# Kernel tuning notes

Measured on AMD Instinct MI355X. Metric: run time of the kernel, lower is better.

## Reference

```python
import jax, jax.numpy as jnp
import numpy as np

NG, ND = 50000, 20000
EG, ED = 300000, 150000
FG = FD = 256
H = 256
FC = 2048
B = 65536
EPS = 1e-5


def _lrelu(x):
    return jnp.where(x >= 0, x, 0.01 * x)


def _bn(x, g, b):
    # BatchNorm1d in training mode: biased batch stats over the node dim
    m = x.mean(axis=0)
    v = ((x - m) ** 2).mean(axis=0)
    return (x - m) * jax.lax.rsqrt(v + EPS) * g + b


def _gconv(x, edge_index, Wr, br, Ws, n_nodes):
    # PyG GraphConv: out = lin_rel(sum_{j->i} x_j) + lin_root(x_i)
    src, dst = edge_index[0], edge_index[1]
    agg = jax.ops.segment_sum(x[src], dst, num_segments=n_nodes)  # [N, in]
    return agg @ Wr + br + x @ Ws


def setup_inputs() -> dict:
    key = jax.random.key(0)
    ks = iter(jax.random.split(key, 64))
    d = {}
    d["gene_x"] = jax.random.normal(next(ks), (NG, FG), jnp.float32)
    d["disease_x"] = jax.random.normal(next(ks), (ND, FD), jnp.float32)
    d["gene_edge_index"] = jax.random.randint(next(ks), (2, EG), 0, NG, jnp.int32)
    d["disease_edge_index"] = jax.random.randint(next(ks), (2, ED), 0, ND, jnp.int32)
    d["batch_idx"] = jax.random.randint(next(ks), (B, 2), 0, ND, jnp.int32)

    def lin(fin, fout):
        s = 1.0 / np.sqrt(fin)
        W = jax.random.uniform(next(ks), (fin, fout), jnp.float32, -s, s)
        b = jax.random.uniform(next(ks), (fout,), jnp.float32, -s, s)
        return W, b

    for p, fin in (("g", FG), ("d", FD)):
        for i in range(3):
            f = fin if i == 0 else H
            Wr, br = lin(f, H)
            Ws, _ = lin(f, H)
            d[f"{p}{i}_Wr"], d[f"{p}{i}_br"], d[f"{p}{i}_Ws"] = Wr, br, Ws
            d[f"bn{p}{i}_g"] = jnp.ones((H,), jnp.float32)
            d[f"bn{p}{i}_b"] = jnp.zeros((H,), jnp.float32)
    d["lin1_W"], d["lin1_b"] = lin(2 * H, FC)
    d["lin2_W"], d["lin2_b"] = lin(FC, FC // 2)
    d["lin3_W"], d["lin3_b"] = lin(FC // 2, FC // 4)
    d["lin4_W"], d["lin4_b"] = lin(FC // 4, 2)
    return d


def reference(gene_x, disease_x, gene_edge_index, disease_edge_index, batch_idx,
              g0_Wr, g0_br, g0_Ws, g1_Wr, g1_br, g1_Ws, g2_Wr, g2_br, g2_Ws,
              d0_Wr, d0_br, d0_Ws, d1_Wr, d1_br, d1_Ws, d2_Wr, d2_br, d2_Ws,
              bng0_g, bng0_b, bng1_g, bng1_b, bng2_g, bng2_b,
              bnd0_g, bnd0_b, bnd1_g, bnd1_b, bnd2_g, bnd2_b,
              lin1_W, lin1_b, lin2_W, lin2_b, lin3_W, lin3_b, lin4_W, lin4_b):
    # gene tower
    g0 = _bn(_lrelu(_gconv(gene_x, gene_edge_index, g0_Wr, g0_br, g0_Ws, NG)), bng0_g, bng0_b)
    g1 = _bn(_lrelu(_gconv(g0, gene_edge_index, g1_Wr, g1_br, g1_Ws, NG)), bng1_g, bng1_b)
    g2 = _bn(_lrelu(_gconv(g1, gene_edge_index, g2_Wr, g2_br, g2_Ws, NG)), bng2_g, bng2_b)
    gene_out = 0.7 * g0 + 0.2 * g1 + 0.1 * g2
    # disease tower
    h0 = _bn(_lrelu(_gconv(disease_x, disease_edge_index, d0_Wr, d0_br, d0_Ws, ND)), bnd0_g, bnd0_b)
    h1 = _bn(_lrelu(_gconv(h0, disease_edge_index, d1_Wr, d1_br, d1_Ws, ND)), bnd1_g, bnd1_b)
    h2 = _bn(_lrelu(_gconv(h1, disease_edge_index, d2_Wr, d2_br, d2_Ws, ND)), bnd2_g, bnd2_b)
    dis_out = 0.7 * h0 + 0.2 * h1 + 0.1 * h2
    # pair gather + MLP head (dropout is identity in eval)
    x = jnp.concatenate([gene_out[batch_idx[:, 0]], dis_out[batch_idx[:, 1]]], axis=1)
    x = _lrelu(x @ lin1_W + lin1_b)
    x = _lrelu(x @ lin2_W + lin2_b)
    x = _lrelu(x @ lin3_W + lin3_b)
    return x @ lin4_W + lin4_b
```

## Files before the change

kernel.cpp:

```cpp
#include <hip/hip_runtime.h>
#include <hip/hip_bf16.h>
#include <cstdint>
#include <cstddef>

#define N_G 50000
#define N_D 20000
#define E_G 300000
#define E_D 150000
#define BATCH 65536

typedef _Float16 f16;
typedef _Float16 f16x8 __attribute__((ext_vector_type(8)));
typedef _Float16 f16x4 __attribute__((ext_vector_type(4)));
typedef float f32x4 __attribute__((ext_vector_type(4)));

__device__ __forceinline__ float clampf(float v) {
    return fminf(fmaxf(v, -60000.f), 60000.f);
}

__device__ __forceinline__ void gl_lds16(const void* g, void* l) {
    __builtin_amdgcn_global_load_lds(
        (const __attribute__((address_space(1))) unsigned int*)g,
        (__attribute__((address_space(3))) unsigned int*)l, 16, 0, 0);
}

__global__ __launch_bounds__(256) void gemm_f16(
    const f16* __restrict__ A,
    const int* __restrict__ bidx,
    const f16* __restrict__ geneT, const f16* __restrict__ disT, int rowBase,
    const f16* __restrict__ Bt, const float* __restrict__ bias,
    f16* __restrict__ C, int M, int N, int K, int relu, int CB, int RB,
    const float* __restrict__ W4, float* __restrict__ outF,
    float* __restrict__ stats)
{
    alignas(16) __shared__ f16 sA[128 * 64];
    alignas(16) __shared__ f16 sB[128 * 64];
    const int t = threadIdx.x;
    const int w = t >> 6, l = t & 63;
    const int wm = w >> 1, wn = w & 1;
    const int q = l >> 4, lr = l & 15;

    int flat = blockIdx.x;
    int cb, rb;
    if ((RB & 7) == 0) {
        int x = flat & 7, idx = flat >> 3;
        int Sx = RB >> 3;
        cb = idx % CB;
        rb = x * Sx + idx / CB;
    } else {
        cb = flat % CB;
        rb = flat / CB;
    }
    const int mBase = rb * 128, nBase = cb * 128;

    const int subrow = l >> 3;
    const int c = l & 7;
    const char* pA[4];
    const char* pD[4];
    const char* pB[4];
    const bool fused = (bidx != nullptr);
    const bool concat = (!fused && disT != nullptr);
    const bool twoSrc = fused || concat;
#pragma unroll
    for (int j = 0; j < 4; j++) {
        int seg = j * 4 + w;
        int lrow = seg * 8 + subrow;
        int coff = ((c ^ (lrow & 7)) << 4);
        if (fused) {
            int rg = rowBase + mBase + lrow;
            int gi = bidx[2 * rg], di = bidx[2 * rg + 1];
            pA[j] = (const char*)geneT + (size_t)gi * 512 + coff;
            pD[j] = (const char*)disT + (size_t)di * 512 + coff;
        } else if (concat) {
            int arow = mBase + lrow; if (arow > M - 1) arow = M - 1;
            pA[j] = (const char*)geneT + (size_t)arow * 512 + coff;
            pD[j] = (const char*)disT + (size_t)arow * 512 + coff;
        } else {
            int arow = mBase + lrow; if (arow > M - 1) arow = M - 1;
            pA[j] = (const char*)A + (size_t)arow * K * 2 + coff;
            pD[j] = nullptr;
        }
        int brow = nBase + lrow; if (brow > N - 1) brow = N - 1;
        pB[j] = (const char*)Bt + (size_t)brow * K * 2 + coff;
    }

    f32x4 acc[4][4] = {};

    for (int k0 = 0; k0 < K; k0 += 64) {
        __syncthreads();
#pragma unroll
        for (int j = 0; j < 4; j++) {
            int seg = j * 4 + w;
            const char* srcA;
            if (twoSrc)
                srcA = (k0 < 256) ? (pA[j] + (size_t)k0 * 2) : (pD[j] + (size_t)(k0 - 256) * 2);
            else
                srcA = pA[j] + (size_t)k0 * 2;
            gl_lds16(srcA, sA + seg * 512);
            gl_lds16(pB[j] + (size_t)k0 * 2, sB + seg * 512);
        }
        __syncthreads();
        f16x8 a0[4], a1[4], b0[4], b1[4];
#pragma unroll
        for (int i = 0; i < 4; i++) {
            int r = wm * 64 + i * 16 + lr;
            int rs = r * 64;
            int x0 = (q ^ (r & 7)) << 3;
            int x1 = ((4 + q) ^ (r & 7)) << 3;
            a0[i] = *(const f16x8*)(sA + rs + x0);
            a1[i] = *(const f16x8*)(sA + rs + x1);
        }
#pragma unroll
        for (int jj = 0; jj < 4; jj++) {
            int r = wn * 64 + jj * 16 + lr;
            int rs = r * 64;
            int x0 = (q ^ (r & 7)) << 3;
            int x1 = ((4 + q) ^ (r & 7)) << 3;
            b0[jj] = *(const f16x8*)(sB + rs + x0);
            b1[jj] = *(const f16x8*)(sB + rs + x1);
        }
#pragma unroll
        for (int i = 0; i < 4; i++)
#pragma unroll
            for (int jj = 0; jj < 4; jj++) {
                acc[i][jj] = __builtin_amdgcn_mfma_f32_16x16x32_f16(a0[i], b0[jj], acc[i][jj], 0, 0, 0);
                acc[i][jj] = __builtin_amdgcn_mfma_f32_16x16x32_f16(a1[i], b1[jj], acc[i][jj], 0, 0, 0);
            }
    }

    if (W4 != nullptr) {
        float w40[4], w41[4];
#pragma unroll
        for (int j = 0; j < 4; j++) {
            int col = nBase + wn * 64 + j * 16 + lr;
            w40[j] = W4[col * 2];
            w41[j] = W4[col * 2 + 1];
        }
#pragma unroll
        for (int i = 0; i < 4; i++) {
#pragma unroll
            for (int r = 0; r < 4; r++) {
                int row = mBase + wm * 64 + i * 16 + q * 4 + r;
                float s0 = 0.f, s1 = 0.f;
#pragma unroll
                for (int j = 0; j < 4; j++) {
                    int col = nBase + wn * 64 + j * 16 + lr;
                    float v = acc[i][j][r] + bias[col];
                    v = v >= 0.f ? v : 0.01f * v;
                    v = clampf(v);
                    s0 += v * w40[j];
                    s1 += v * w41[j];
                }
#pragma unroll
                for (int off = 1; off < 16; off <<= 1) {
                    s0 += __shfl_xor(s0, off);
                    s1 += __shfl_xor(s1, off);
                }
                if (lr == 0 && row < M) {
                    atomicAdd(&outF[(size_t)(rowBase + row) * 2], s0);
                    atomicAdd(&outF[(size_t)(rowBase + row) * 2 + 1], s1);
                }
            }
        }
        return;
    }

    __syncthreads();
    f16* lt = ((w >> 1) ? sB : sA) + (w & 1) * 4096;

    float bj[4];
#pragma unroll
    for (int j = 0; j < 4; j++)
        bj[j] = bias ? bias[nBase + wn * 64 + j * 16 + lr] : 0.f;

    float sj[4] = {0.f, 0.f, 0.f, 0.f}, s2j[4] = {0.f, 0.f, 0.f, 0.f};
#pragma unroll
    for (int i = 0; i < 4; i++)
#pragma unroll
        for (int j = 0; j < 4; j++) {
            int col = j * 16 + lr;
#pragma unroll
            for (int r = 0; r < 4; r++) {
                int row = i * 16 + q * 4 + r;
                float v = acc[i][j][r] + bj[j];
                if (relu) v = v >= 0.f ? v : 0.01f * v;
                v = clampf(v);
                if (stats && (mBase + wm * 64 + row) < M) { sj[j] += v; s2j[j] += v * v; }
                int cs = col ^ ((((row >> 2) & 3) << 4) ^ ((row & 3) << 3));
                lt[row * 64 + cs] = (f16)v;
            }
        }

    if (stats) {
#pragma unroll
        for (int j = 0; j < 4; j++) {
            float s = sj[j], s2 = s2j[j];
            s += __shfl_xor(s, 16); s2 += __shfl_xor(s2, 16);
            s += __shfl_xor(s, 32); s2 += __shfl_xor(s2, 32);
            if (q == 0) {
                int col = nBase + wn * 64 + j * 16 + lr;
                if (col < 256 && col < N) {
                    atomicAdd(&stats[col], s);
                    atomicAdd(&stats[256 + col], s2);
                }
            }
        }
    }
    __syncthreads();

    const int rr = l >> 3;
    const int c8 = l & 7;
#pragma unroll
    for (int it = 0; it < 8; it++) {
        int row = it * 8 + rr;
        int cs = (c8 * 8) ^ ((((row >> 2) & 3) << 4) ^ ((row & 3) << 3));
        f16x8 vv = *(const f16x8*)(lt + row * 64 + cs);
        int grow = mBase + wm * 64 + row;
        if (grow < M)
            *(f16x8*)(C + (size_t)grow * N + nBase + wn * 64 + c8 * 8) = vv;
    }
}

__global__ __launch_bounds__(512) void gemm256(
    const f16* __restrict__ A,
    const int* __restrict__ bidx,
    const f16* __restrict__ geneT, const f16* __restrict__ disT, int rowBase,
    const f16* __restrict__ Bt, const float* __restrict__ bias,
    f16* __restrict__ C, int M, int N, int K, int relu, int CB, int RB)
{
    alignas(16) __shared__ f16 sm[81920];
    const int t = threadIdx.x;
    const int w = t >> 6, l = t & 63;
    const int wm = w >> 2, wn = w & 3;
    const int q = l >> 4, lr = l & 15;

    int flat = blockIdx.x;
    int cb, rb;
    if ((RB & 7) == 0) {
        int x = flat & 7, idx = flat >> 3;
        int Sx = RB >> 3;
        cb = idx % CB;
        rb = x * Sx + idx / CB;
    } else {
        cb = flat % CB;
        rb = flat / CB;
    }
    const int mBase = rb * 256, nBase = cb * 256;

    const int subrow = l >> 3;
    const int c = l & 7;
    const bool gat = (bidx != nullptr);
    const char* pA[4];
    const char* pD[4];
    const char* pB[4];
#pragma unroll
    for (int jj = 0; jj < 4; jj++) {
        int arow = jj * 64 + w * 8 + subrow;
        int coff = ((c ^ (arow & 7)) << 4);
        if (gat) {
            int rg = rowBase + mBase + arow;
            int gi = bidx[2 * rg], di = bidx[2 * rg + 1];
            pA[jj] = (const char*)geneT + (size_t)gi * 512 + coff;
            pD[jj] = (const char*)disT + (size_t)di * 512 + coff;
        } else {
            int ga = mBase + arow; if (ga > M - 1) ga = M - 1;
            pA[jj] = (const char*)A + (size_t)ga * K * 2 + coff;
            pD[jj] = nullptr;
        }
        int gb = nBase + arow; if (gb > N - 1) gb = N - 1;
        pB[jj] = (const char*)Bt + (size_t)gb * K * 2 + coff;
    }

    f16* const smA = sm;
    f16* const smB = sm + 3 * 16384;

    auto stageA = [&](int abuf, int k0) {
        f16* bA = smA + abuf * 16384;
#pragma unroll
        for (int jj = 0; jj < 4; jj++) {
            int R0 = jj * 64 + w * 8;
            const char* srcA;
            if (gat)
                srcA = (k0 < 256) ? (pA[jj] + (size_t)k0 * 2) : (pD[jj] + (size_t)(k0 - 256) * 2);
            else
                srcA = pA[jj] + (size_t)k0 * 2;
            gl_lds16(srcA, bA + R0 * 64);
        }
    };
    auto stageB = [&](int bbuf, int k0) {
        f16* bB = smB + bbuf * 16384;
#pragma unroll
        for (int jj = 0; jj < 4; jj++) {
            int R0 = jj * 64 + w * 8;
            gl_lds16(pB[jj] + (size_t)k0 * 2, bB + R0 * 64);
        }
    };

    f32x4 acc[8][4] = {};
    const int nkt = K >> 6;

    stageA(0, 0);
    stageB(0, 0);
    if (nkt > 1) stageA(1, 64);

    for (int kt = 0; kt < nkt; kt++) {
        if (kt + 1 < nkt) stageB((kt + 1) & 1, (kt + 1) << 6);
        if (kt + 2 < nkt) stageA((kt + 2) % 3, (kt + 2) << 6);
        if (kt + 2 < nkt)      asm volatile("s_waitcnt vmcnt(12)" ::: "memory");
        else if (kt + 1 < nkt) asm volatile("s_waitcnt vmcnt(8)" ::: "memory");
        else                   asm volatile("s_waitcnt vmcnt(0)" ::: "memory");
        __builtin_amdgcn_s_barrier();
        __builtin_amdgcn_sched_barrier(0);
        const f16* bA = smA + (kt % 3) * 16384;
        const f16* bB = smB + (kt & 1) * 16384;
#pragma unroll
        for (int ks = 0; ks < 2; ks++) {
            f16x8 bf[4];
#pragma unroll
            for (int nf = 0; nf < 4; nf++) {
                int rB = wn * 64 + nf * 16 + lr;
                bf[nf] = *(const f16x8*)(bB + rB * 64 + ((((ks << 2) + q) ^ (rB & 7)) << 3));
            }
#pragma unroll
            for (int mf = 0; mf < 8; mf++) {
                int rA = wm * 128 + mf * 16 + lr;
                f16x8 af = *(const f16x8*)(bA + rA * 64 + ((((ks << 2) + q) ^ (rA & 7)) << 3));
#pragma unroll
                for (int nf = 0; nf < 4; nf++)
                    acc[mf][nf] = __builtin_amdgcn_mfma_f32_16x16x32_f16(af, bf[nf], acc[mf][nf], 0, 0, 0);
            }
        }
        __builtin_amdgcn_sched_barrier(0);
        __builtin_amdgcn_s_barrier();
    }
    __builtin_amdgcn_sched_barrier(0);

    f16* lt = sm + w * 8192;
    float bj[4];
#pragma unroll
    for (int nf = 0; nf < 4; nf++)
        bj[nf] = bias ? bias[nBase + wn * 64 + nf * 16 + lr] : 0.f;

#pragma unroll
    for (int mf = 0; mf < 8; mf++)
#pragma unroll
        for (int nf = 0; nf < 4; nf++) {
            int col = nf * 16 + lr;
#pragma unroll
            for (int r = 0; r < 4; r++) {
                int row = mf * 16 + q * 4 + r;
                float v = acc[mf][nf][r] + bj[nf];
                if (relu) v = v >= 0.f ? v : 0.01f * v;
                v = clampf(v);
                int cs = col ^ ((((row >> 2) & 3) << 4) ^ ((row & 3) << 3));
                lt[row * 64 + cs] = (f16)v;
            }
        }

    const int rr = l >> 3;
    const int c8 = l & 7;
#pragma unroll
    for (int it = 0; it < 16; it++) {
        int row = it * 8 + rr;
        int cs = (c8 * 8) ^ ((((row >> 2) & 3) << 4) ^ ((row & 3) << 3));
        f16x8 vv = *(const f16x8*)(lt + row * 64 + cs);
        int grow = mBase + wm * 128 + row;
        if (grow < M)
            *(f16x8*)(C + (size_t)grow * N + nBase + wn * 64 + c8 * 8) = vv;
    }
}

__global__ void cvt_f32_f16(const float* __restrict__ in, f16* __restrict__ out, size_t n) {
    size_t i = ((size_t)blockIdx.x * 256 + threadIdx.x) * 8;
    if (i >= n) return;
    f32x4 a = *(const f32x4*)(in + i);
    f32x4 b = *(const f32x4*)(in + i + 4);
    f16x8 o;
    o[0] = (f16)clampf(a.x); o[1] = (f16)clampf(a.y);
    o[2] = (f16)clampf(a.z); o[3] = (f16)clampf(a.w);
    o[4] = (f16)clampf(b.x); o[5] = (f16)clampf(b.y);
    o[6] = (f16)clampf(b.z); o[7] = (f16)clampf(b.w);
    *(f16x8*)(out + i) = o;
}

__global__ void init_out(const float* __restrict__ b4, float* __restrict__ out, int n) {
    int i = blockIdx.x * 256 + threadIdx.x;
    if (i < n) out[i] = b4[i & 1];
}

__global__ void count_deg(const int* __restrict__ ei, int E, int* __restrict__ deg) {
    int e = blockIdx.x * 256 + threadIdx.x;
    if (e < E) atomicAdd(&deg[ei[E + e]], 1);
}

__global__ void scan_deg(const int* __restrict__ deg, int* __restrict__ rowptr, int Nn) {
    __shared__ int part[1024];
    const int t = threadIdx.x;
    const int C = (Nn + 1023) >> 10;
    const int base = t * C;
    int s = 0;
    for (int i = 0; i < C; i++) { int idx = base + i; if (idx < Nn) s += deg[idx]; }
    part[t] = s;
    __syncthreads();
    for (int off = 1; off < 1024; off <<= 1) {
        int v = (t >= off) ? part[t - off] : 0;
        __syncthreads();
        part[t] += v;
        __syncthreads();
    }
    int pre = (t == 0) ? 0 : part[t - 1];
    for (int i = 0; i < C; i++) {
        int idx = base + i;
        if (idx < Nn) { rowptr[idx] = pre; pre += deg[idx]; }
    }
    if (t == 1023) rowptr[Nn] = part[1023];
}

__global__ void fill_csr(const int* __restrict__ ei, int E, const int* __restrict__ rowptr,
                         int* __restrict__ cursor, int* __restrict__ csr) {
    int e = blockIdx.x * 256 + threadIdx.x;
    if (e < E) {
        int d = ei[E + e];
        int p = rowptr[d] + atomicAdd(&cursor[d], 1);
        csr[p] = ei[e];
    }
}

__global__ void agg_x(const int* __restrict__ rowptr, const int* __restrict__ csr,
                      const f16* __restrict__ X, f16* __restrict__ XA, int Nn) {
    int gid = blockIdx.x * 256 + threadIdx.x;
    int node = gid >> 6, l = gid & 63;
    if (node >= Nn) return;
    int beg = rowptr[node], end = rowptr[node + 1];
    float s0 = 0.f, s1 = 0.f, s2 = 0.f, s3 = 0.f;
    for (int e = beg; e < end; e++) {
        int src = csr[e];
        f16x4 xv = *(const f16x4*)(X + (size_t)src * 256 + l * 4);
        s0 += (float)xv.x; s1 += (float)xv.y; s2 += (float)xv.z; s3 += (float)xv.w;
    }
    f16x4 o;
    o.x = (f16)clampf(s0); o.y = (f16)clampf(s1);
    o.z = (f16)clampf(s2); o.w = (f16)clampf(s3);
    *(f16x4*)(XA + (size_t)node * 256 + l * 4) = o;
}

__global__ void transpose_tile(const float* __restrict__ W, f16* __restrict__ WT,
                               int K, int N, int dstRowOff, int dstColOff, int LK) {
    __shared__ float tile[32][33];
    int n0 = blockIdx.x * 32, k0 = blockIdx.y * 32;
    int tx = threadIdx.x, ty = threadIdx.y;
    for (int yy = ty; yy < 32; yy += 8) {
        int k = k0 + yy, n = n0 + tx;
        tile[yy][tx] = (k < K && n < N) ? W[(size_t)k * N + n] : 0.f;
    }
    __syncthreads();
    for (int yy = ty; yy < 32; yy += 8) {
        int n = n0 + yy, k = k0 + tx;
        if (n < N && k < K)
            WT[(size_t)(dstRowOff + n) * LK + dstColOff + k] = (f16)clampf(tile[tx][yy]);
    }
}

__global__ void bn_apply(f16* __restrict__ y, const float* __restrict__ stats,
                         const float* __restrict__ g, const float* __restrict__ b,
                         float invN, float w, f16* __restrict__ acc, size_t total,
                         int initAcc) {
    size_t i = ((size_t)blockIdx.x * 256 + threadIdx.x) * 8;
    if (i >= total) return;
    int colb = (int)(i & 255);
    f16x8 yv = *(const f16x8*)(y + i);
    f16x8 av = {};
    if (!initAcc) av = *(const f16x8*)(acc + i);
    f16x8 yo, ao;
#pragma unroll
    for (int j = 0; j < 8; j++) {
        int col = colb + j;
        float m = stats[col] * invN;
        float var = stats[256 + col] * invN - m * m;
        if (var < 0.f) var = 0.f;
        float rs = 1.0f / sqrtf(var + 1e-5f);
        float v = ((float)yv[j] - m) * rs * g[col] + b[col];
        v = clampf(v);
        yo[j] = (f16)v;
        float p = initAcc ? 0.f : (float)av[j];
        ao[j] = (f16)clampf(p + w * v);
    }
    *(f16x8*)(y + i) = yo;
    *(f16x8*)(acc + i) = ao;
}

extern "C" void kernel_launch(void* const* d_in, const int* in_sizes, int n_in,
                              void* d_out, int out_size, void* d_ws, size_t ws_size,
                              hipStream_t stream) {
    char* ws = (char*)d_ws;
    size_t off = 0;
    auto alloc = [&](size_t bytes) -> void* {
        void* p = ws + off;
        off += (bytes + 255) & ~(size_t)255;
        return p;
    };

    f16* gene_out = (f16*)alloc((size_t)N_G * 256 * 2);
    f16* dis_out  = (f16*)alloc((size_t)N_D * 256 * 2);
    f16* W1T = (f16*)alloc((size_t)2048 * 512 * 2);
    f16* W2T = (f16*)alloc((size_t)1024 * 2048 * 2);
    f16* W3T = (f16*)alloc((size_t)512 * 1024 * 2);
    f16* WcatT = (f16*)alloc((size_t)256 * 512 * 2);
    int* csr = (int*)alloc((size_t)E_G * 4);
    int* rowptr = (int*)alloc((size_t)(N_G + 1) * 4);
    int* cnt = (int*)alloc((size_t)N_G * 4);
    float* stats = (float*)alloc(512 * 4);

    char* scratch = ws + off;
    size_t avail = (ws_size > off) ? (ws_size - off) : 0;

    f16* ybA = (f16*)scratch;
    f16* ybB = ybA + (size_t)N_G * 256;
    f16* XAbuf = ybB + (size_t)N_G * 256;

    int R = 32768;
    while ((size_t)R * 6144 > avail && R > 256) R >>= 1;
    int chunks = BATCH / R;
    f16* h1 = (f16*)scratch;
    f16* h2 = h1 + (size_t)R * 2048;

    const float* gene_x = (const float*)d_in[0];
    const float* disease_x = (const float*)d_in[1];
    const int* g_ei = (const int*)d_in[2];
    const int* d_ei = (const int*)d_in[3];
    const int* bidx = (const int*)d_in[4];
    float* out = (float*)d_out;

    const float wl[3] = {0.7f, 0.2f, 0.1f};

    auto run_tower = [&](const float* xin, const int* ei, int Nn, int E, int pbase, f16* tout) {
        size_t nelem = (size_t)Nn * 256;
        cvt_f32_f16<<<(int)((nelem / 8 + 255) / 256), 256, 0, stream>>>(xin, ybA, nelem);
        hipMemsetAsync(cnt, 0, (size_t)Nn * 4, stream);
        count_deg<<<(E + 255) / 256, 256, 0, stream>>>(ei, E, cnt);
        scan_deg<<<1, 1024, 0, stream>>>(cnt, rowptr, Nn);
        hipMemsetAsync(cnt, 0, (size_t)Nn * 4, stream);
        fill_csr<<<(E + 255) / 256, 256, 0, stream>>>(ei, E, rowptr, cnt, csr);
        f16* yin = ybA;
        f16* yout = ybB;
        int RB = (Nn + 127) / 128;
        int RBp = (RB + 7) & ~7;
        for (int l = 0; l < 3; l++) {
            const float* Wr = (const float*)d_in[pbase + l * 5 + 0];
            const float* br = (const float*)d_in[pbase + l * 5 + 1];
            const float* Wss = (const float*)d_in[pbase + l * 5 + 2];
            const float* bg = (const float*)d_in[pbase + l * 5 + 3];
            const float* bb = (const float*)d_in[pbase + l * 5 + 4];
            transpose_tile<<<dim3(8, 8), dim3(32, 8), 0, stream>>>(Wss, WcatT, 256, 256, 0, 0, 512);
            transpose_tile<<<dim3(8, 8), dim3(32, 8), 0, stream>>>(Wr, WcatT, 256, 256, 0, 256, 512);
            agg_x<<<(Nn * 64 + 255) / 256, 256, 0, stream>>>(rowptr, csr, yin, XAbuf, Nn);
            hipMemsetAsync(stats, 0, 512 * 4, stream);
            gemm_f16<<<2 * RBp, 256, 0, stream>>>(nullptr, nullptr, yin, XAbuf, 0,
                                                  WcatT, br, yout, Nn, 256, 512, 1, 2, RBp,
                                                  nullptr, nullptr, stats);
            bn_apply<<<(int)((nelem / 8 + 255) / 256), 256, 0, stream>>>(
                yout, stats, bg, bb, 1.0f / Nn, wl[l], tout, nelem, l == 0);
            f16* tmp = yin; yin = yout; yout = tmp;
        }
    };

    run_tower(gene_x, g_ei, N_G, E_G, 5, gene_out);
    run_tower(disease_x, d_ei, N_D, E_D, 20, dis_out);

    const float* lin1_W = (const float*)d_in[35];
    const float* lin1_b = (const float*)d_in[36];
    const float* lin2_W = (const float*)d_in[37];
    const float* lin2_b = (const float*)d_in[38];
    const float* lin3_W = (const float*)d_in[39];
    const float* lin3_b = (const float*)d_in[40];
    const float* lin4_W = (const float*)d_in[41];
    const float* lin4_b = (const float*)d_in[42];

    transpose_tile<<<dim3(64, 16), dim3(32, 8), 0, stream>>>(lin1_W, W1T, 512, 2048, 0, 0, 512);
    transpose_tile<<<dim3(32, 64), dim3(32, 8), 0, stream>>>(lin2_W, W2T, 2048, 1024, 0, 0, 2048);
    transpose_tile<<<dim3(16, 32), dim3(32, 8), 0, stream>>>(lin3_W, W3T, 1024, 512, 0, 0, 1024);
    init_out<<<(BATCH * 2 + 255) / 256, 256, 0, stream>>>(lin4_b, out, BATCH * 2);

    for (int c = 0; c < chunks; c++) {
        int rb = c * R;
        if ((R & 255) == 0) {
            int RB2 = R / 256;
            gemm256<<<8 * RB2, 512, 0, stream>>>(nullptr, bidx, gene_out, dis_out, rb,
                                                 W1T, lin1_b, h1, R, 2048, 512, 1, 8, RB2);
            gemm256<<<4 * RB2, 512, 0, stream>>>(h1, nullptr, nullptr, nullptr, 0,
                                                 W2T, lin2_b, h2, R, 1024, 2048, 1, 4, RB2);
        } else {
            int RB = R / 128;
            gemm_f16<<<16 * RB, 256, 0, stream>>>(nullptr, bidx, gene_out, dis_out, rb,
                                                  W1T, lin1_b, h1, R, 2048, 512, 1, 16, RB,
                                                  nullptr, nullptr, nullptr);
            gemm_f16<<<8 * RB, 256, 0, stream>>>(h1, nullptr, nullptr, nullptr, 0,
                                                 W2T, lin2_b, h2, R, 1024, 2048, 1, 8, RB,
                                                 nullptr, nullptr, nullptr);
        }
        int RB = R / 128;
        gemm_f16<<<4 * RB, 256, 0, stream>>>(h2, nullptr, nullptr, nullptr, rb,
                                             W3T, lin3_b, nullptr, R, 512, 1024, 1, 4, RB,
                                             lin4_W, out, nullptr);
    }
}
```

Measured before the change: 1.467 ms.

## Add dedicated tower GEMM kernel and use 128-tile GEMM for MLP layer 2

Moves the BatchNorm statistics epilogue out of the general gemm_f16 into a new specialized gemm_tower kernel for the graph-conv layers. gemm_tower reads the root and aggregated features directly and always applies bias, leaky ReLU and the stats reduction, so the shared kernel no longer carries those branches. The second MLP layer now always uses the 128x128 gemm_f16 instead of the 256-row gemm256 kernel. This trades larger-tile reuse for a different occupancy and grid shape on the largest GEMM.

```diff
diff --git a/kernel.cpp b/kernel.cpp
--- a/kernel.cpp
+++ b/kernel.cpp
@@ -30,8 +30,7 @@
     const f16* __restrict__ geneT, const f16* __restrict__ disT, int rowBase,
     const f16* __restrict__ Bt, const float* __restrict__ bias,
     f16* __restrict__ C, int M, int N, int K, int relu, int CB, int RB,
-    const float* __restrict__ W4, float* __restrict__ outF,
-    float* __restrict__ stats)
+    const float* __restrict__ W4, float* __restrict__ outF)
 {
     alignas(16) __shared__ f16 sA[128 * 64];
     alignas(16) __shared__ f16 sB[128 * 64];
@@ -173,7 +172,6 @@
     for (int j = 0; j < 4; j++)
         bj[j] = bias ? bias[nBase + wn * 64 + j * 16 + lr] : 0.f;
 
-    float sj[4] = {0.f, 0.f, 0.f, 0.f}, s2j[4] = {0.f, 0.f, 0.f, 0.f};
 #pragma unroll
     for (int i = 0; i < 4; i++)
 #pragma unroll
@@ -185,27 +183,10 @@
                 float v = acc[i][j][r] + bj[j];
                 if (relu) v = v >= 0.f ? v : 0.01f * v;
                 v = clampf(v);
-                if (stats && (mBase + wm * 64 + row) < M) { sj[j] += v; s2j[j] += v * v; }
                 int cs = col ^ ((((row >> 2) & 3) << 4) ^ ((row & 3) << 3));
                 lt[row * 64 + cs] = (f16)v;
             }
         }
-
-    if (stats) {
-#pragma unroll
-        for (int j = 0; j < 4; j++) {
-            float s = sj[j], s2 = s2j[j];
-            s += __shfl_xor(s, 16); s2 += __shfl_xor(s2, 16);
-            s += __shfl_xor(s, 32); s2 += __shfl_xor(s2, 32);
-            if (q == 0) {
-                int col = nBase + wn * 64 + j * 16 + lr;
-                if (col < 256 && col < N) {
-                    atomicAdd(&stats[col], s);
-                    atomicAdd(&stats[256 + col], s2);
-                }
-            }
-        }
-    }
     __syncthreads();
 
     const int rr = l >> 3;
@@ -365,6 +346,144 @@
         int cs = (c8 * 8) ^ ((((row >> 2) & 3) << 4) ^ ((row & 3) << 3));
         f16x8 vv = *(const f16x8*)(lt + row * 64 + cs);
         int grow = mBase + wm * 128 + row;
+        if (grow < M)
+            *(f16x8*)(C + (size_t)grow * N + nBase + wn * 64 + c8 * 8) = vv;
+    }
+}
+
+__global__ __launch_bounds__(256) void gemm_tower(
+    const f16* __restrict__ X, const f16* __restrict__ XA,
+    const f16* __restrict__ Bt, const float* __restrict__ bias,
+    f16* __restrict__ C, int M, int N, int K, int CB, int RB,
+    float* __restrict__ stats)
+{
+    alignas(16) __shared__ f16 sA[128 * 64];
+    alignas(16) __shared__ f16 sB[128 * 64];
+    const int t = threadIdx.x;
+    const int w = t >> 6, l = t & 63;
+    const int wm = w >> 1, wn = w & 1;
+    const int q = l >> 4, lr = l & 15;
+
+    int flat = blockIdx.x;
+    int cb, rb;
+    if ((RB & 7) == 0) {
+        int x = flat & 7, idx = flat >> 3;
+        int Sx = RB >> 3;
+        cb = idx % CB;
+        rb = x * Sx + idx / CB;
+    } else {
+        cb = flat % CB;
+        rb = flat / CB;
+    }
+    const int mBase = rb * 128, nBase = cb * 128;
+
+    const int subrow = l >> 3;
+    const int c = l & 7;
+    const char* pA[4];
+    const char* pD[4];
+    const char* pB[4];
+#pragma unroll
+    for (int j = 0; j < 4; j++) {
+        int seg = j * 4 + w;
+        int lrow = seg * 8 + subrow;
+        int coff = ((c ^ (lrow & 7)) << 4);
+        int arow = mBase + lrow; if (arow > M - 1) arow = M - 1;
+        pA[j] = (const char*)X + (size_t)arow * 512 + coff;
+        pD[j] = (const char*)XA + (size_t)arow * 512 + coff;
+        int brow = nBase + lrow; if (brow > N - 1) brow = N - 1;
+        pB[j] = (const char*)Bt + (size_t)brow * K * 2 + coff;
+    }
+
+    f32x4 acc[4][4] = {};
+
+    for (int k0 = 0; k0 < K; k0 += 64) {
+        __syncthreads();
+#pragma unroll
+        for (int j = 0; j < 4; j++) {
+            int seg = j * 4 + w;
+            const char* srcA = (k0 < 256) ? (pA[j] + (size_t)k0 * 2)
+                                          : (pD[j] + (size_t)(k0 - 256) * 2);
+            gl_lds16(srcA, sA + seg * 512);
+            gl_lds16(pB[j] + (size_t)k0 * 2, sB + seg * 512);
+        }
+        __syncthreads();
+        f16x8 a0[4], a1[4], b0[4], b1[4];
+#pragma unroll
+        for (int i = 0; i < 4; i++) {
+            int r = wm * 64 + i * 16 + lr;
+            int rs = r * 64;
+            int x0 = (q ^ (r & 7)) << 3;
+            int x1 = ((4 + q) ^ (r & 7)) << 3;
+            a0[i] = *(const f16x8*)(sA + rs + x0);
+            a1[i] = *(const f16x8*)(sA + rs + x1);
+        }
+#pragma unroll
+        for (int jj = 0; jj < 4; jj++) {
+            int r = wn * 64 + jj * 16 + lr;
+            int rs = r * 64;
+            int x0 = (q ^ (r & 7)) << 3;
+            int x1 = ((4 + q) ^ (r & 7)) << 3;
+            b0[jj] = *(const f16x8*)(sB + rs + x0);
+            b1[jj] = *(const f16x8*)(sB + rs + x1);
+        }
+#pragma unroll
+        for (int i = 0; i < 4; i++)
+#pragma unroll
+            for (int jj = 0; jj < 4; jj++) {
+                acc[i][jj] = __builtin_amdgcn_mfma_f32_16x16x32_f16(a0[i], b0[jj], acc[i][jj], 0, 0, 0);
+                acc[i][jj] = __builtin_amdgcn_mfma_f32_16x16x32_f16(a1[i], b1[jj], acc[i][jj], 0, 0, 0);
+            }
+    }
+
+    __syncthreads();
+    f16* lt = ((w >> 1) ? sB : sA) + (w & 1) * 4096;
+
+    float bj[4];
+#pragma unroll
+    for (int j = 0; j < 4; j++)
+        bj[j] = bias[nBase + wn * 64 + j * 16 + lr];
+
+    float sj[4] = {0.f, 0.f, 0.f, 0.f}, s2j[4] = {0.f, 0.f, 0.f, 0.f};
+#pragma unroll
+    for (int i = 0; i < 4; i++)
+#pragma unroll
+        for (int j = 0; j < 4; j++) {
+            int col = j * 16 + lr;
+#pragma unroll
+            for (int r = 0; r < 4; r++) {
+                int row = i * 16 + q * 4 + r;
+                float v = acc[i][j][r] + bj[j];
+                v = v >= 0.f ? v : 0.01f * v;
+                v = clampf(v);
+                if ((mBase + wm * 64 + row) < M) { sj[j] += v; s2j[j] += v * v; }
+                int cs = col ^ ((((row >> 2) & 3) << 4) ^ ((row & 3) << 3));
+                lt[row * 64 + cs] = (f16)v;
+            }
+        }
+
+#pragma unroll
+    for (int j = 0; j < 4; j++) {
+        float s = sj[j], s2 = s2j[j];
+        s += __shfl_xor(s, 16); s2 += __shfl_xor(s2, 16);
+        s += __shfl_xor(s, 32); s2 += __shfl_xor(s2, 32);
+        if (q == 0) {
+            int col = nBase + wn * 64 + j * 16 + lr;
+            if (col < N) {
+                atomicAdd(&stats[col], s);
+                atomicAdd(&stats[256 + col], s2);
+            }
+        }
+    }
+    __syncthreads();
+
+    const int rr = l >> 3;
+    const int c8 = l & 7;
+#pragma unroll
+    for (int it = 0; it < 8; it++) {
+        int row = it * 8 + rr;
+        int cs = (c8 * 8) ^ ((((row >> 2) & 3) << 4) ^ ((row & 3) << 3));
+        f16x8 vv = *(const f16x8*)(lt + row * 64 + cs);
+        int grow = mBase + wm * 64 + row;
         if (grow < M)
             *(f16x8*)(C + (size_t)grow * N + nBase + wn * 64 + c8 * 8) = vv;
     }
@@ -535,7 +654,8 @@
 
     auto run_tower = [&](const float* xin, const int* ei, int Nn, int E, int pbase, f16* tout) {
         size_t nelem = (size_t)Nn * 256;
-        cvt_f32_f16<<<(int)((nelem / 8 + 255) / 256), 256, 0, stream>>>(xin, ybA, nelem);
+        int nb8 = (int)((nelem / 8 + 255) / 256);
+        cvt_f32_f16<<<nb8, 256, 0, stream>>>(xin, ybA, nelem);
         hipMemsetAsync(cnt, 0, (size_t)Nn * 4, stream);
         count_deg<<<(E + 255) / 256, 256, 0, stream>>>(ei, E, cnt);
         scan_deg<<<1, 1024, 0, stream>>>(cnt, rowptr, Nn);
@@ -555,11 +675,10 @@
             transpose_tile<<<dim3(8, 8), dim3(32, 8), 0, stream>>>(Wr, WcatT, 256, 256, 0, 256, 512);
             agg_x<<<(Nn * 64 + 255) / 256, 256, 0, stream>>>(rowptr, csr, yin, XAbuf, Nn);
             hipMemsetAsync(stats, 0, 512 * 4, stream);
-            gemm_f16<<<2 * RBp, 256, 0, stream>>>(nullptr, nullptr, yin, XAbuf, 0,
-                                                  WcatT, br, yout, Nn, 256, 512, 1, 2, RBp,
-                                                  nullptr, nullptr, stats);
-            bn_apply<<<(int)((nelem / 8 + 255) / 256), 256, 0, stream>>>(
-                yout, stats, bg, bb, 1.0f / Nn, wl[l], tout, nelem, l == 0);
+            gemm_tower<<<2 * RBp, 256, 0, stream>>>(yin, XAbuf, WcatT, br, yout,
+                                                    Nn, 256, 512, 2, RBp, stats);
+            bn_apply<<<nb8, 256, 0, stream>>>(yout, stats, bg, bb, 1.0f / Nn, wl[l],
+                                              tout, nelem, l == 0);
             f16* tmp = yin; yin = yout; yout = tmp;
         }
     };
@@ -583,24 +702,21 @@
 
     for (int c = 0; c < chunks; c++) {
         int rb = c * R;
+        int RB = R / 128;
         if ((R & 255) == 0) {
             int RB2 = R / 256;
             gemm256<<<8 * RB2, 512, 0, stream>>>(nullptr, bidx, gene_out, dis_out, rb,
                                                  W1T, lin1_b, h1, R, 2048, 512, 1, 8, RB2);
-            gemm256<<<4 * RB2, 512, 0, stream>>>(h1, nullptr, nullptr, nullptr, 0,
-                                                 W2T, lin2_b, h2, R, 1024, 2048, 1, 4, RB2);
         } else {
-            int RB = R / 128;
             gemm_f16<<<16 * RB, 256, 0, stream>>>(nullptr, bidx, gene_out, dis_out, rb,
                                                   W1T, lin1_b, h1, R, 2048, 512, 1, 16, RB,
-                                                  nullptr, nullptr, nullptr);
-            gemm_f16<<<8 * RB, 256, 0, stream>>>(h1, nullptr, nullptr, nullptr, 0,
-                                                 W2T, lin2_b, h2, R, 1024, 2048, 1, 8, RB,
-                                                 nullptr, nullptr, nullptr);
-        }
-        int RB = R / 128;
+                                                  nullptr, nullptr);
+        }
+        gemm_f16<<<8 * RB, 256, 0, stream>>>(h1, nullptr, nullptr, nullptr, 0,
+                                             W2T, lin2_b, h2, R, 1024, 2048, 1, 8, RB,
+                                             nullptr, nullptr);
         gemm_f16<<<4 * RB, 256, 0, stream>>>(h2, nullptr, nullptr, nullptr, rb,
                                              W3T, lin3_b, nullptr, R, 512, 1024, 1, 4, RB,
-                                             lin4_W, out, nullptr);
-    }
-}
+                                             lin4_W, out);
+    }
+}
```

Result: slower. 1.557 ms (+6.1%).
